# Kernel tuning notes

Measured on AMD Instinct MI355X. Metric: run time of the kernel, lower is better.

The kernel has to match this reference:

```python
import jax, jax.numpy as jnp
import numpy as np

B, S, E, H, MLP = 2, 2048, 1024, 16, 4096
VEC = 8          # args.vec_length: block-row height of vector-sparse mask
SPARSITY = 0.9   # fraction of attention entries dropped
D = E // H


def _make_mask():
    # static_random_mask_aligned: each block-row of VEC query rows keeps a
    # random ~(1-sparsity) subset of key columns. Diagonal kept so every
    # softmax row is non-empty.
    rng = np.random.default_rng(0)
    block = rng.random((S // VEC, S)) < (1.0 - SPARSITY)   # [m, n]
    mask = np.repeat(block, VEC, axis=0)                   # [S, S]
    mask |= np.eye(S, dtype=bool)
    return jnp.asarray(mask)


def setup_inputs() -> dict:
    key = jax.random.key(0)
    ks = jax.random.split(key, 8)
    w = lambda k, shp: (0.02 * jax.random.normal(k, shp, dtype=jnp.float32))
    return {
        "x": jax.random.normal(ks[0], (B, S, E), dtype=jnp.float32),
        "mask": _make_mask(),                       # [S,S] bool, static
        "w_qkv": w(ks[1], (3 * E, E)),             # in_proj_weight
        "b_qkv": jnp.zeros((3 * E,), jnp.float32),
        "w_out": w(ks[2], (E, E)),                 # out_proj
        "b_out": jnp.zeros((E,), jnp.float32),
        "g1": jnp.ones((E,), jnp.float32), "beta1": jnp.zeros((E,), jnp.float32),
        "g2": jnp.ones((E,), jnp.float32), "beta2": jnp.zeros((E,), jnp.float32),
        "w1": w(ks[3], (MLP, E)), "bias1": jnp.zeros((MLP,), jnp.float32),
        "w2": w(ks[4], (E, MLP)), "bias2": jnp.zeros((E,), jnp.float32),
    }


def _layer_norm(x, g, b, eps=1e-5):
    mu = jnp.mean(x, axis=-1, keepdims=True)
    var = jnp.mean(jnp.square(x - mu), axis=-1, keepdims=True)
    return (x - mu) * jax.lax.rsqrt(var + eps) * g + b


def _sparse_mha(h, mask, w_qkv, b_qkv, w_out, b_out):
    qkv = jnp.einsum("bse,fe->bsf", h, w_qkv) + b_qkv       # [B,S,3E]
    q, k, v = jnp.split(qkv, 3, axis=-1)
    q = q.reshape(B, S, H, D)
    k = k.reshape(B, S, H, D)
    v = v.reshape(B, S, H, D)
    scores = jnp.einsum("bqhd,bkhd->bhqk", q, k) / jnp.sqrt(jnp.float32(D))
    scores = jnp.where(mask[None, None], scores, jnp.float32(-1e9))
    p = jax.nn.softmax(scores, axis=-1)
    ctx = jnp.einsum("bhqk,bkhd->bqhd", p, v).reshape(B, S, E)
    return jnp.einsum("bse,fe->bsf", ctx, w_out) + b_out


def reference(x, mask, w_qkv, b_qkv, w_out, b_out, g1, beta1, g2, beta2,
              w1, bias1, w2, bias2):
    h = _layer_norm(x, g1, beta1)
    attn = _sparse_mha(h, mask, w_qkv, b_qkv, w_out, b_out)
    out = attn + x                      # residual 1
    out = _layer_norm(out, g2, beta2)
    out = jnp.einsum("bse,me->bsm", out, w1) + bias1   # linear1 (no activation, as in source)
    out = jnp.einsum("bsm,em->bse", out, w2) + bias2   # linear2
    return out + x                      # residual adds ORIGINAL x (as in source)
```

## Files before the change

### kernel.cpp

```cpp
#include <hip/hip_runtime.h>
#include <cstdint>
#include <cstddef>

typedef unsigned short u16;
typedef unsigned int u32;
typedef unsigned long long u64;
typedef short s16x8 __attribute__((ext_vector_type(8)));
typedef float f32x4 __attribute__((ext_vector_type(4)));
typedef _Float16 f16x4 __attribute__((ext_vector_type(4)));
typedef _Float16 f16x8 __attribute__((ext_vector_type(8)));

#define S_LEN 2048
#define EMB   1024
#define NHEAD 16
#define HD    64
#define E3    3072
#define MLPD  4096
#define NROWS 4096
#define LCAP  640

__device__ __forceinline__ float bf2f(u16 v) {
  union { u32 i; float f; } c; c.i = ((u32)v) << 16; return c.f;
}
__device__ __forceinline__ u16 f2bf(float f) {
  union { float f; u32 i; } c; c.f = f;
  u32 x = c.i;
  return (u16)((x + 0x7FFFu + ((x >> 16) & 1u)) >> 16);
}
__device__ __forceinline__ u16 f2h(float f) {
  _Float16 h = (_Float16)f;
  union { _Float16 h; u16 b; } c; c.h = h; return c.b;
}

__device__ __forceinline__ void gl2lds16(const void* g, void* l) {
  __builtin_amdgcn_global_load_lds(
      (__attribute__((address_space(1))) void*)(g),
      (__attribute__((address_space(3))) void*)(l), 16, 0, 0);
}

__global__ void detect_flags(const u32* __restrict__ w1s, int* __restrict__ dtflag,
                             const u32* __restrict__ mask, int* __restrict__ maskrep) {
  __shared__ int hits[256];
  __shared__ u32 red[256];
  int h = 0; u32 v = 0;
  for (int i = threadIdx.x; i < 4096; i += 256) {
    u32 w = w1s[i];
    if ((w & 0xFFFFu) && (((w >> 7) & 0xFFu) >= 0xC8u)) ++h;
    v |= mask[i];
  }
  hits[threadIdx.x] = h; red[threadIdx.x] = v;
  __syncthreads();
  if (threadIdx.x == 0) {
    int t = 0; u32 o = 0;
    for (int i = 0; i < 256; ++i) { t += hits[i]; o |= red[i]; }
    *dtflag = (t > 8) ? 1 : 0;
    int rep;
    if (o <= 1u) rep = 0;
    else if (o & 0x80u) rep = 1;
    else if (o & 0x00800000u) rep = 2;
    else rep = 3;
    *maskrep = rep;
  }
}

__device__ __forceinline__ bool maskbit(const void* m, int rep, size_t idx) {
  switch (rep) {
    case 0:  return ((const int*)m)[idx] != 0;
    case 1:  return ((const u16*)m)[idx] != 0;
    case 2:  return ((const u32*)m)[idx] != 0;
    default: return ((const unsigned char*)m)[idx] != 0;
  }
}

__global__ __launch_bounds__(256)
void cvt_kernel(const void* __restrict__ src, u16* __restrict__ dst,
                int n8, const int* __restrict__ dtflag) {
  const int i = blockIdx.x * blockDim.x + threadIdx.x;
  if (i >= n8) return;
  if (*dtflag) {
    const float4 a = ((const float4*)src)[i * 2];
    const float4 b = ((const float4*)src)[i * 2 + 1];
    u16 o[8] = {f2bf(a.x), f2bf(a.y), f2bf(a.z), f2bf(a.w),
                f2bf(b.x), f2bf(b.y), f2bf(b.z), f2bf(b.w)};
    *(uint4*)(dst + (size_t)i * 8) = *(const uint4*)o;
  } else {
    ((uint4*)dst)[i] = ((const uint4*)src)[i];
  }
}

__global__ void cvt_small(const void* s0, u16* d0, const void* s1, u16* d1,
                          const void* s2, u16* d2, const void* s3, u16* d3,
                          const void* s4, u16* d4, const void* s5, u16* d5,
                          const void* s6, u16* d6, const void* s7, u16* d7,
                          const int* __restrict__ dtflag) {
  const int f = *dtflag;
  const void* srcs[8] = {s0, s1, s2, s3, s4, s5, s6, s7};
  u16* dsts[8] = {d0, d1, d2, d3, d4, d5, d6, d7};
  const int ns[8] = {E3, EMB, EMB, EMB, EMB, EMB, MLPD, EMB};
#pragma unroll
  for (int k = 0; k < 8; ++k) {
    for (int idx = threadIdx.x; idx < ns[k]; idx += 256)
      dsts[k][idx] = f ? f2bf(((const float*)srcs[k])[idx])
                       : ((const u16*)srcs[k])[idx];
  }
}

__global__ void build_lists(const void* __restrict__ mask, const int* __restrict__ repf,
                            int* __restrict__ lists, int* __restrict__ cnt,
                            unsigned char* __restrict__ diagflag) {
  __shared__ int num;
  const int m = blockIdx.x;
  if (threadIdx.x == 0) num = 0;
  __syncthreads();
  const int rep = *repf;
  const int row0 = m * 8;
  for (int j = threadIdx.x; j < S_LEN; j += 256) {
    int srcrow = (j == row0) ? (row0 + 1) : row0;
    bool bit = maskbit(mask, rep, (size_t)srcrow * S_LEN + j);
    if (j >= row0 && j < row0 + 8) diagflag[j] = bit ? 0 : 1;
    if (bit) {
      int p = atomicAdd(&num, 1);
      if (p < LCAP) lists[m * LCAP + p] = j * 256;
    }
  }
  __syncthreads();
  if (threadIdx.x == 0) cnt[m] = (num < LCAP) ? num : LCAP;
}

__global__ __launch_bounds__(256)
void ln_kernel(const void* __restrict__ Xv, const u16* __restrict__ g,
               const u16* __restrict__ be, u16* __restrict__ O,
               const int* __restrict__ inf32) {
  const int wv = threadIdx.x >> 6, ln = threadIdx.x & 63;
  const int row = blockIdx.x * 4 + wv;
  float v[16];
  if (inf32 && *inf32) {
    const float* xr = (const float*)Xv + (size_t)row * EMB;
    float4 a0 = *(const float4*)(xr + ln * 8);
    float4 a1 = *(const float4*)(xr + ln * 8 + 4);
    float4 b0 = *(const float4*)(xr + 512 + ln * 8);
    float4 b1 = *(const float4*)(xr + 512 + ln * 8 + 4);
    v[0]=a0.x; v[1]=a0.y; v[2]=a0.z; v[3]=a0.w; v[4]=a1.x; v[5]=a1.y; v[6]=a1.z; v[7]=a1.w;
    v[8]=b0.x; v[9]=b0.y; v[10]=b0.z; v[11]=b0.w; v[12]=b1.x; v[13]=b1.y; v[14]=b1.z; v[15]=b1.w;
  } else {
    const u16* xr = (const u16*)Xv + (size_t)row * EMB;
    union { uint4 u; u16 s[8]; } p0, p1;
    p0.u = *(const uint4*)(xr + ln * 8);
    p1.u = *(const uint4*)(xr + 512 + ln * 8);
#pragma unroll
    for (int t = 0; t < 8; ++t) { v[t] = bf2f(p0.s[t]); v[8 + t] = bf2f(p1.s[t]); }
  }
  float s = 0.f, sq = 0.f;
#pragma unroll
  for (int t = 0; t < 16; ++t) { s += v[t]; sq += v[t] * v[t]; }
#pragma unroll
  for (int off = 32; off; off >>= 1) { s += __shfl_xor(s, off); sq += __shfl_xor(sq, off); }
  const float mu = s * (1.0f / EMB);
  const float var = sq * (1.0f / EMB) - mu * mu;
  const float rsig = rsqrtf(var + 1e-5f);
  union { uint4 u; u16 s[8]; } g0, g1v, b0, b1v, o0, o1;
  g0.u = *(const uint4*)(g + ln * 8);   g1v.u = *(const uint4*)(g + 512 + ln * 8);
  b0.u = *(const uint4*)(be + ln * 8);  b1v.u = *(const uint4*)(be + 512 + ln * 8);
#pragma unroll
  for (int t = 0; t < 8; ++t) {
    o0.s[t] = f2bf((v[t]     - mu) * rsig * bf2f(g0.s[t])  + bf2f(b0.s[t]));
    o1.s[t] = f2bf((v[8 + t] - mu) * rsig * bf2f(g1v.s[t]) + bf2f(b1v.s[t]));
  }
  u16* orow = O + (size_t)row * EMB;
  *(uint4*)(orow + ln * 8) = o0.u;
  *(uint4*)(orow + 512 + ln * 8) = o1.u;
}

__global__ __launch_bounds__(256)
void gemm_bt(const u16* __restrict__ A, const u16* __restrict__ B,
             const u16* __restrict__ bias, u16* __restrict__ C,
             int M, int N, int K) {
  __shared__ u16 a_sh[128 * 64];
  __shared__ u16 b_sh[128 * 64];
  const int tid = threadIdx.x;
  const int wv = tid >> 6, ln = tid & 63;
  const int wm = wv & 1, wn = wv >> 1;
  const int tm = blockIdx.y, tn = blockIdx.x;
  const int srow = ln >> 3;
  const int scol = ((ln & 7) ^ srow) * 8;
  const int q = ln >> 4, rr = ln & 15;

  f32x4 acc[4][4] = {};
  const u16* Abase = A + (size_t)(tm * 128) * K;
  const u16* Bbase = B + (size_t)(tn * 128) * K;

  for (int k0 = 0; k0 < K; k0 += 64) {
    __syncthreads();
#pragma unroll
    for (int c = 0; c < 4; ++c) {
      const int chunk = wv * 4 + c;
      const int row = chunk * 8 + srow;
      gl2lds16(Abase + (size_t)row * K + k0 + scol, &a_sh[chunk * 512]);
      gl2lds16(Bbase + (size_t)row * K + k0 + scol, &b_sh[chunk * 512]);
    }
    __syncthreads();
#pragma unroll
    for (int kk = 0; kk < 2; ++kk) {
      const int slot = ((kk * 4 + q) ^ (rr & 7)) * 8;
      s16x8 af[4], bfr[4];
#pragma unroll
      for (int mi = 0; mi < 4; ++mi)
        af[mi] = *(const s16x8*)&a_sh[(wm * 64 + mi * 16 + rr) * 64 + slot];
#pragma unroll
      for (int ni = 0; ni < 4; ++ni)
        bfr[ni] = *(const s16x8*)&b_sh[(wn * 64 + ni * 16 + rr) * 64 + slot];
#pragma unroll
      for (int mi = 0; mi < 4; ++mi)
#pragma unroll
        for (int ni = 0; ni < 4; ++ni)
          acc[mi][ni] = __builtin_amdgcn_mfma_f32_16x16x32_bf16(af[mi], bfr[ni], acc[mi][ni], 0, 0, 0);
    }
  }
#pragma unroll
  for (int ni = 0; ni < 4; ++ni) {
    const int col = tn * 128 + wn * 64 + ni * 16 + rr;
    const float bv = bf2f(bias[col]);
#pragma unroll
    for (int mi = 0; mi < 4; ++mi)
#pragma unroll
      for (int r2 = 0; r2 < 4; ++r2) {
        const int row = tm * 128 + wm * 64 + mi * 16 + q * 4 + r2;
        C[(size_t)row * N + col] = f2bf(acc[mi][ni][r2] + bv);
      }
  }
}

__global__ __launch_bounds__(256)
void gemm_bt_sk(const u16* __restrict__ A, const u16* __restrict__ B,
                u16* __restrict__ P0, u16* __restrict__ P1,
                int M, int N, int K) {
  __shared__ u16 a_sh[128 * 64];
  __shared__ u16 b_sh[128 * 64];
  const int tid = threadIdx.x;
  const int wv = tid >> 6, ln = tid & 63;
  const int wm = wv & 1, wn = wv >> 1;
  const int tm = blockIdx.y, tn = blockIdx.x, kz = blockIdx.z;
  const int Kh = K >> 1;
  const int koff = kz * Kh;
  const int srow = ln >> 3;
  const int scol = ((ln & 7) ^ srow) * 8;
  const int q = ln >> 4, rr = ln & 15;

  f32x4 acc[4][4] = {};
  const u16* Abase = A + (size_t)(tm * 128) * K + koff;
  const u16* Bbase = B + (size_t)(tn * 128) * K + koff;

  for (int k0 = 0; k0 < Kh; k0 += 64) {
    __syncthreads();
#pragma unroll
    for (int c = 0; c < 4; ++c) {
      const int chunk = wv * 4 + c;
      const int row = chunk * 8 + srow;
      gl2lds16(Abase + (size_t)row * K + k0 + scol, &a_sh[chunk * 512]);
      gl2lds16(Bbase + (size_t)row * K + k0 + scol, &b_sh[chunk * 512]);
    }
    __syncthreads();
#pragma unroll
    for (int kk = 0; kk < 2; ++kk) {
      const int slot = ((kk * 4 + q) ^ (rr & 7)) * 8;
      s16x8 af[4], bfr[4];
#pragma unroll
      for (int mi = 0; mi < 4; ++mi)
        af[mi] = *(const s16x8*)&a_sh[(wm * 64 + mi * 16 + rr) * 64 + slot];
#pragma unroll
      for (int ni = 0; ni < 4; ++ni)
        bfr[ni] = *(const s16x8*)&b_sh[(wn * 64 + ni * 16 + rr) * 64 + slot];
#pragma unroll
      for (int mi = 0; mi < 4; ++mi)
#pragma unroll
        for (int ni = 0; ni < 4; ++ni)
          acc[mi][ni] = __builtin_amdgcn_mfma_f32_16x16x32_bf16(af[mi], bfr[ni], acc[mi][ni], 0, 0, 0);
    }
  }
  u16* P = kz ? P1 : P0;
#pragma unroll
  for (int ni = 0; ni < 4; ++ni) {
    const int col = tn * 128 + wn * 64 + ni * 16 + rr;
#pragma unroll
    for (int mi = 0; mi < 4; ++mi)
#pragma unroll
      for (int r2 = 0; r2 < 4; ++r2) {
        const int row = tm * 128 + wm * 64 + mi * 16 + q * 4 + r2;
        P[(size_t)row * N + col] = f2bf(acc[mi][ni][r2]);
      }
  }
}

__global__ __launch_bounds__(256)
void combine_kernel(const u16* __restrict__ P0, const u16* __restrict__ P1,
                    const u16* __restrict__ bias, const void* __restrict__ xr,
                    void* __restrict__ Ov, const int* __restrict__ f32io) {
  const int i = blockIdx.x * 256 + threadIdx.x;
  const int col8 = (i & 127) * 8;
  union { uint4 u; u16 s[8]; } a, b, bi;
  a.u = ((const uint4*)P0)[i];
  b.u = ((const uint4*)P1)[i];
  bi.u = *(const uint4*)(bias + col8);
  const int f = *f32io;
  float o[8];
#pragma unroll
  for (int t = 0; t < 8; ++t) o[t] = bf2f(a.s[t]) + bf2f(b.s[t]) + bf2f(bi.s[t]);
  if (f) {
    const float4 x0 = ((const float4*)xr)[i * 2];
    const float4 x1 = ((const float4*)xr)[i * 2 + 1];
    o[0]+=x0.x; o[1]+=x0.y; o[2]+=x0.z; o[3]+=x0.w;
    o[4]+=x1.x; o[5]+=x1.y; o[6]+=x1.z; o[7]+=x1.w;
    float4 r0 = {o[0],o[1],o[2],o[3]}, r1 = {o[4],o[5],o[6],o[7]};
    ((float4*)Ov)[i * 2] = r0;
    ((float4*)Ov)[i * 2 + 1] = r1;
  } else {
    union { uint4 u; u16 s[8]; } xv;
    xv.u = ((const uint4*)xr)[i];
    u16 r[8];
#pragma unroll
    for (int t = 0; t < 8; ++t) r[t] = f2bf(o[t] + bf2f(xv.s[t]));
    ((uint4*)Ov)[i] = *(const uint4*)r;
  }
}

__global__ __launch_bounds__(256)
void gemm_qkv(const u16* __restrict__ A, const u16* __restrict__ B,
              const u16* __restrict__ bias,
              u16* __restrict__ Qb, u16* __restrict__ KVp,
              int K) {
  __shared__ u16 a_sh[128 * 64];
  __shared__ u16 b_sh[128 * 64];
  const int tid = threadIdx.x;
  const int wv = tid >> 6, ln = tid & 63;
  const int wm = wv & 1, wn = wv >> 1;
  const int tm = blockIdx.y, tn = blockIdx.x;
  const int srow = ln >> 3;
  const int scol = ((ln & 7) ^ srow) * 8;
  const int q = ln >> 4, rr = ln & 15;

  f32x4 acc[4][4] = {};
  const u16* Abase = A + (size_t)(tm * 128) * K;
  const u16* Bbase = B + (size_t)(tn * 128) * K;

  for (int k0 = 0; k0 < K; k0 += 64) {
    __syncthreads();
#pragma unroll
    for (int c = 0; c < 4; ++c) {
      const int chunk = wv * 4 + c;
      const int row = chunk * 8 + srow;
      gl2lds16(Abase + (size_t)row * K + k0 + scol, &a_sh[chunk * 512]);
      gl2lds16(Bbase + (size_t)row * K + k0 + scol, &b_sh[chunk * 512]);
    }
    __syncthreads();
#pragma unroll
    for (int kk = 0; kk < 2; ++kk) {
      const int slot = ((kk * 4 + q) ^ (rr & 7)) * 8;
      s16x8 af[4], bfr[4];
#pragma unroll
      for (int mi = 0; mi < 4; ++mi)
        af[mi] = *(const s16x8*)&a_sh[(wm * 64 + mi * 16 + rr) * 64 + slot];
#pragma unroll
      for (int ni = 0; ni < 4; ++ni)
        bfr[ni] = *(const s16x8*)&b_sh[(wn * 64 + ni * 16 + rr) * 64 + slot];
#pragma unroll
      for (int mi = 0; mi < 4; ++mi)
#pragma unroll
        for (int ni = 0; ni < 4; ++ni)
          acc[mi][ni] = __builtin_amdgcn_mfma_f32_16x16x32_bf16(af[mi], bfr[ni], acc[mi][ni], 0, 0, 0);
    }
  }
  const int third = (tn * 128) >> 10;
  const float QS = 0.125f * 1.44269504f;
#pragma unroll
  for (int ni = 0; ni < 4; ++ni) {
    const int col = tn * 128 + wn * 64 + ni * 16 + rr;
    const int w = col & 1023;
    const float bv = bf2f(bias[col]);
#pragma unroll
    for (int mi = 0; mi < 4; ++mi)
#pragma unroll
      for (int r2 = 0; r2 < 4; ++r2) {
        const int row = tm * 128 + wm * 64 + mi * 16 + q * 4 + r2;
        const float o = acc[mi][ni][r2] + bv;
        if (third == 0) {
          Qb[(size_t)row * 1024 + w] = f2h(o * QS);
        } else {
          const int hh = w >> 6, d = w & 63;
          const int bq_ = row >> 11, s = row & 2047;
          KVp[((size_t)(bq_ * NHEAD + hh) * S_LEN + s) * 128 +
              ((third == 1) ? 0 : 64) + d] = f2h(o);
        }
      }
  }
}

__global__ __launch_bounds__(256)
void gemm_bt_n64(const u16* __restrict__ A, const u16* __restrict__ B,
                 const u16* __restrict__ bias, const void* __restrict__ resid,
                 void* __restrict__ Cv, int M, int N, int K,
                 const int* __restrict__ residf32, const int* __restrict__ outf32) {
  __shared__ u16 a_sh[128 * 64];
  __shared__ u16 b_sh[64 * 64];
  const int tid = threadIdx.x;
  const int wv = tid >> 6, ln = tid & 63;
  const int wm = wv & 1, wn = wv >> 1;
  const int tm = blockIdx.y, tn = blockIdx.x;
  const int srow = ln >> 3;
  const int scol = ((ln & 7) ^ srow) * 8;
  const int q = ln >> 4, rr = ln & 15;

  f32x4 acc[4][2] = {};
  const u16* Abase = A + (size_t)(tm * 128) * K;
  const u16* Bbase = B + (size_t)(tn * 64) * K;

  for (int k0 = 0; k0 < K; k0 += 64) {
    __syncthreads();
#pragma unroll
    for (int c = 0; c < 4; ++c) {
      const int chunk = wv * 4 + c;
      const int row = chunk * 8 + srow;
      gl2lds16(Abase + (size_t)row * K + k0 + scol, &a_sh[chunk * 512]);
    }
#pragma unroll
    for (int c = 0; c < 2; ++c) {
      const int chunk = wv * 2 + c;
      const int row = chunk * 8 + srow;
      gl2lds16(Bbase + (size_t)row * K + k0 + scol, &b_sh[chunk * 512]);
    }
    __syncthreads();
#pragma unroll
    for (int kk = 0; kk < 2; ++kk) {
      const int slot = ((kk * 4 + q) ^ (rr & 7)) * 8;
      s16x8 af[4], bfr[2];
#pragma unroll
      for (int mi = 0; mi < 4; ++mi)
        af[mi] = *(const s16x8*)&a_sh[(wm * 64 + mi * 16 + rr) * 64 + slot];
#pragma unroll
      for (int ni = 0; ni < 2; ++ni)
        bfr[ni] = *(const s16x8*)&b_sh[(wn * 32 + ni * 16 + rr) * 64 + slot];
#pragma unroll
      for (int mi = 0; mi < 4; ++mi)
#pragma unroll
        for (int ni = 0; ni < 2; ++ni)
          acc[mi][ni] = __builtin_amdgcn_mfma_f32_16x16x32_bf16(af[mi], bfr[ni], acc[mi][ni], 0, 0, 0);
    }
  }
  const int rf32 = residf32 ? *residf32 : 0;
  const int f32o = outf32 ? *outf32 : 0;
#pragma unroll
  for (int ni = 0; ni < 2; ++ni) {
    const int col = tn * 64 + wn * 32 + ni * 16 + rr;
    const float bv = bf2f(bias[col]);
#pragma unroll
    for (int mi = 0; mi < 4; ++mi)
#pragma unroll
      for (int r2 = 0; r2 < 4; ++r2) {
        const int row = tm * 128 + wm * 64 + mi * 16 + q * 4 + r2;
        const size_t idx = (size_t)row * N + col;
        float o = acc[mi][ni][r2] + bv;
        if (resid)
          o += rf32 ? ((const float*)resid)[idx] : bf2f(((const u16*)resid)[idx]);
        if (f32o) ((float*)Cv)[idx] = o;
        else      ((u16*)Cv)[idx] = f2bf(o);
      }
  }
}

__global__ __launch_bounds__(256)
void attn_kernel(const u16* __restrict__ Qb, const u16* __restrict__ KVp,
                 const int* __restrict__ lists,
                 const int* __restrict__ cnt, const unsigned char* __restrict__ diagflag,
                 u16* __restrict__ ctx) {
  __shared__ int list_sh[4][LCAP];
  __shared__ uint4 vsh4[4][128];
  const int g = blockIdx.x;
  const int bh = g & 31;
  const int mq = g >> 5;
  const int b = bh >> 4, h = bh & 15;
  const int tid = threadIdx.x, wv = tid >> 6, ln = tid & 63;
  const int lg = ln >> 4;
  const int dl = ln & 15;
  const int m = mq * 4 + wv;
  const int i0 = m * 8;

#pragma unroll
  for (int w = 0; w < 4; ++w) {
    const int nw = cnt[mq * 4 + w];
    for (int e = tid; e < nw; e += 256) list_sh[w][e] = lists[(mq * 4 + w) * LCAP + e];
  }
  __syncthreads();

  const int n = cnt[m];
  const u64 du = *(const u64*)(diagflag + i0);

  f16x8 qb0 = {}, qb1 = {};
  if (dl < 8) {
    const u16* qr = Qb + (size_t)(b * S_LEN + i0 + dl) * EMB + h * 64 + lg * 8;
    union { uint4 u; f16x8 h; } a0, a1;
    a0.u = *(const uint4*)qr;
    a1.u = *(const uint4*)(qr + 32);
    qb0 = a0.h; qb1 = a1.h;
  }

  const char* kvb = (const char*)KVp + (size_t)bh * S_LEN * 256;

  uint4* vwp = &vsh4[wv][0];
  const int widx = ((lg >> 1) << 5) + ((dl & 3) << 3) + ((dl >> 2) << 1) + (lg & 1);
  const u16* vrp = (const u16*)vwp + (lg << 4) + dl;

  float rs = 0.f;
  f32x4 acc[4] = {};

  auto CHUNK = [&](int c0, int mode) {
    int le;
    if (mode == 2) {
      le = (i0 + (dl & 7)) * 256;
    } else {
      const int e = c0 + dl;
      const int idx = (mode == 1 && e >= n) ? 0 : e;
      le = list_sh[wv][idx];
    }
    const char* base = kvb + le + (lg << 4);
    union { uint4 u; f16x8 h; } ka0, ka1;
    ka0.u = *(const uint4*)(base);
    ka1.u = *(const uint4*)(base + 64);
    const uint4 v0 = *(const uint4*)(base + 128);
    const uint4 v1 = *(const uint4*)(base + 192);

    f32x4 st = {};
    st = __builtin_amdgcn_mfma_f32_16x16x32_f16(ka0.h, qb0, st, 0, 0, 0);
    st = __builtin_amdgcn_mfma_f32_16x16x32_f16(ka1.h, qb1, st, 0, 0, 0);

    vwp[widx] = v0;
    vwp[widx + 64] = v1;

    _Float16 ph[4];
#pragma unroll
    for (int r = 0; r < 4; ++r) {
      float s = st[r];
      s = fminf(fmaxf(s, -126.f), 15.f);
      float p = exp2f(s);
      bool keep = true;
      const int e2 = (lg << 2) + r;
      if (mode == 1) keep = (c0 + e2) < n;
      if (mode == 2) keep = (e2 == dl) && (((du >> ((e2 & 7) * 8)) & 1ull) != 0ull);
      p = keep ? p : 0.f;
      ph[r] = (_Float16)p;
      rs += (float)ph[r];
    }
    const f16x4 pa = { ph[0], ph[1], ph[2], ph[3] };

#pragma unroll
    for (int dc = 0; dc < 4; ++dc) {
      union { u16 s[4]; f16x4 h; } bf;
      bf.s[0] = vrp[dc * 256 +   0];
      bf.s[1] = vrp[dc * 256 +  64];
      bf.s[2] = vrp[dc * 256 + 128];
      bf.s[3] = vrp[dc * 256 + 192];
      acc[dc] = __builtin_amdgcn_mfma_f32_16x16x16f16(pa, bf.h, acc[dc], 0, 0, 0);
    }
  };

  int c0 = 0;
  for (; c0 + 16 <= n; c0 += 16) CHUNK(c0, 0);
  if (c0 < n) CHUNK(c0, 1);
  CHUNK(0, 2);

  rs += __shfl_xor(rs, 16);
  rs += __shfl_xor(rs, 32);

  float invs[4];
#pragma unroll
  for (int r = 0; r < 4; ++r) invs[r] = __shfl(rs, (lg << 2) + r);

  if (lg < 2) {
#pragma unroll
    for (int r = 0; r < 4; ++r) {
      const float inv = 1.0f / invs[r];
      u16* orow = ctx + (size_t)(b * S_LEN + i0 + (lg << 2) + r) * EMB + h * 64 + dl;
#pragma unroll
      for (int dc = 0; dc < 4; ++dc)
        orow[dc * 16] = f2bf(acc[dc][r] * inv);
    }
  }
}

extern "C" void kernel_launch(void* const* d_in, const int* in_sizes, int n_in,
                              void* d_out, int out_size, void* d_ws, size_t ws_size,
                              hipStream_t stream) {
  const void* x_raw    = d_in[0];
  const void* mask     = d_in[1];
  const void* wqkv_raw = d_in[2];
  const void* bqkv_raw = d_in[3];
  const void* wout_raw = d_in[4];
  const void* bout_raw = d_in[5];
  const void* g1_raw   = d_in[6];
  const void* be1_raw  = d_in[7];
  const void* g2_raw   = d_in[8];
  const void* be2_raw  = d_in[9];
  const void* w1_raw   = d_in[10];
  const void* b1_raw   = d_in[11];
  const void* w2_raw   = d_in[12];
  const void* b2_raw   = d_in[13];

  char* ws = (char*)d_ws;
  const size_t MB = 1u << 20;
  int* dtflag         = (int*)ws;
  int* maskrep        = (int*)(ws + 64);
  int* cnt            = (int*)(ws + 1024);
  unsigned char* dfl  = (unsigned char*)(ws + 4096);
  int* lists          = (int*)(ws + 8192);
  u16* R1  = (u16*)(ws + 1 * MB);
  u16* Qb  = (u16*)(ws + 9 * MB);
  u16* KVp = (u16*)(ws + 17 * MB);
  u16* M1  = (u16*)(ws + 17 * MB);
  u16* W   = (u16*)(ws + 49 * MB);
  char* sm = ws + 57 * MB;
  u16* bq  = (u16*)(sm);
  u16* bo  = (u16*)(sm + 8192);
  u16* g1b = (u16*)(sm + 16384);
  u16* be1b= (u16*)(sm + 24576);
  u16* g2b = (u16*)(sm + 32768);
  u16* be2b= (u16*)(sm + 40960);
  u16* b1b = (u16*)(sm + 49152);
  u16* b2b = (u16*)(sm + 65536);

  detect_flags<<<dim3(1), dim3(256), 0, stream>>>((const u32*)w1_raw, dtflag,
                                                  (const u32*)mask, maskrep);
  build_lists<<<dim3(256), dim3(256), 0, stream>>>(mask, maskrep, lists, cnt, dfl);
  cvt_small<<<dim3(1), dim3(256), 0, stream>>>(
      bqkv_raw, bq, bout_raw, bo, g1_raw, g1b, be1_raw, be1b,
      g2_raw, g2b, be2_raw, be2b, b1_raw, b1b, b2_raw, b2b, dtflag);

  auto cvt = [&](const void* src, u16* dst, int n) {
    const int n8 = n / 8;
    cvt_kernel<<<dim3((n8 + 255) / 256), dim3(256), 0, stream>>>(src, dst, n8, dtflag);
  };

  ln_kernel<<<dim3(NROWS / 4), dim3(256), 0, stream>>>(x_raw, g1b, be1b, R1, dtflag);
  cvt(wqkv_raw, W, E3 * EMB);
  gemm_qkv<<<dim3(E3 / 128, NROWS / 128), dim3(256), 0, stream>>>(
      R1, W, bq, Qb, KVp, EMB);
  attn_kernel<<<dim3(2 * NHEAD * 64), dim3(256), 0, stream>>>(
      Qb, KVp, lists, cnt, dfl, R1);
  cvt(wout_raw, W, EMB * EMB);
  gemm_bt_n64<<<dim3(EMB / 64, NROWS / 128), dim3(256), 0, stream>>>(
      R1, W, bo, x_raw, Qb, NROWS, EMB, EMB, dtflag, nullptr);
  ln_kernel<<<dim3(NROWS / 4), dim3(256), 0, stream>>>(Qb, g2b, be2b, R1, nullptr);
  cvt(w1_raw, W, MLPD * EMB);
  gemm_bt<<<dim3(MLPD / 128, NROWS / 128), dim3(256), 0, stream>>>(
      R1, W, b1b, M1, NROWS, MLPD, EMB);
  cvt(w2_raw, W, EMB * MLPD);
  gemm_bt_sk<<<dim3(EMB / 128, NROWS / 128, 2), dim3(256), 0, stream>>>(
      M1, W, R1, Qb, NROWS, EMB, MLPD);
  combine_kernel<<<dim3(NROWS * EMB / 8 / 256), dim3(256), 0, stream>>>(
      R1, Qb, b2b, x_raw, d_out, dtflag);
}
```

Measured before the change: 411.6 us.

## Software-pipeline sparse attention gathers with double-buffered swizzled V tiles

Restructures the attention chunk loop so the K/V gather for the next 16-key chunk is issued into registers before the current chunk's MFMAs run. The V tile is double-buffered in LDS with a new swizzled layout, which removes the load-to-use stall on each scattered global read. Key lists are stored as 16-bit indices with a smaller cap, and a 6-waves occupancy hint is added, both to shrink LDS and raise residency. The trade-off is higher register pressure from the prefetch registers, and the kernel now assumes no block-row has more than 320 kept keys.

```diff
diff --git a/kernel.cpp b/kernel.cpp
--- a/kernel.cpp
+++ b/kernel.cpp
@@ -17,7 +17,7 @@
 #define E3    3072
 #define MLPD  4096
 #define NROWS 4096
-#define LCAP  640
+#define LCAP  320
 
 __device__ __forceinline__ float bf2f(u16 v) {
   union { u32 i; float f; } c; c.i = ((u32)v) << 16; return c.f;
@@ -466,13 +466,13 @@
   }
 }
 
-__global__ __launch_bounds__(256)
+__global__ __launch_bounds__(256, 6)
 void attn_kernel(const u16* __restrict__ Qb, const u16* __restrict__ KVp,
                  const int* __restrict__ lists,
                  const int* __restrict__ cnt, const unsigned char* __restrict__ diagflag,
                  u16* __restrict__ ctx) {
-  __shared__ int list_sh[4][LCAP];
-  __shared__ uint4 vsh4[4][128];
+  __shared__ u16 list_sh[4][LCAP];
+  __shared__ uint4 vsh4[4][2][128];
   const int g = blockIdx.x;
   const int bh = g & 31;
   const int mq = g >> 5;
@@ -486,7 +486,8 @@
 #pragma unroll
   for (int w = 0; w < 4; ++w) {
     const int nw = cnt[mq * 4 + w];
-    for (int e = tid; e < nw; e += 256) list_sh[w][e] = lists[(mq * 4 + w) * LCAP + e];
+    for (int e = tid; e < nw; e += 256)
+      list_sh[w][e] = (u16)((u32)lists[(mq * 4 + w) * LCAP + e] >> 8);
   }
   __syncthreads();
 
@@ -504,67 +505,99 @@
 
   const char* kvb = (const char*)KVp + (size_t)bh * S_LEN * 256;
 
-  uint4* vwp = &vsh4[wv][0];
-  const int widx = ((lg >> 1) << 5) + ((dl & 3) << 3) + ((dl >> 2) << 1) + (lg & 1);
-  const u16* vrp = (const u16*)vwp + (lg << 4) + dl;
+  const int wslab = ((dl >> 2) & 1)
+                  + ((((dl >> 1) & 1) ^ (dl >> 3)) << 1)
+                  + (((dl & 1) ^ (lg & 1)) << 2)
+                  + ((dl >> 3) << 3)
+                  + ((lg & 1) << 4)
+                  + (((lg >> 1) & 1) << 5);
+  const int c3l = lg >> 1, o0l = dl >> 3;
+  const int LB = ((lg & 1) << 3) + (c3l << 6) + (o0l << 7) + (dl & 7);
+  const int tm0 = ((0 ^ c3l) << 4) + ((0 ^ o0l) << 5);
+  const int tm1 = ((0 ^ c3l) << 4) + ((1 ^ o0l) << 5);
+  const int tm2 = ((1 ^ c3l) << 4) + ((1 ^ o0l) << 5) - ((1 ^ o0l) << 5) + ((0 ^ o0l) << 5);
+  const int tm3 = ((1 ^ c3l) << 4) + ((1 ^ o0l) << 5);
+  const u16* vtile = (const u16*)&vsh4[wv][0][0];
 
   float rs = 0.f;
   f32x4 acc[4] = {};
-
-  auto CHUNK = [&](int c0, int mode) {
+  const int T = ((n + 15) >> 4) + 1;
+
+  auto kaddr = [&](int ci) -> const char* {
     int le;
-    if (mode == 2) {
-      le = (i0 + (dl & 7)) * 256;
+    if (ci >= T - 1) {
+      le = (i0 + (dl & 7)) << 8;
     } else {
-      const int e = c0 + dl;
-      const int idx = (mode == 1 && e >= n) ? 0 : e;
-      le = list_sh[wv][idx];
-    }
-    const char* base = kvb + le + (lg << 4);
-    union { uint4 u; f16x8 h; } ka0, ka1;
-    ka0.u = *(const uint4*)(base);
-    ka1.u = *(const uint4*)(base + 64);
-    const uint4 v0 = *(const uint4*)(base + 128);
-    const uint4 v1 = *(const uint4*)(base + 192);
-
+      const int e = ci * 16 + dl;
+      le = ((int)list_sh[wv][(e < n) ? e : 0]) << 8;
+    }
+    return kvb + le + (lg << 4);
+  };
+
+  uint4 ka0, ka1;
+  {
+    const char* p0 = kaddr(0);
+    ka0 = *(const uint4*)p0;
+    ka1 = *(const uint4*)(p0 + 64);
+    const uint4 w0 = *(const uint4*)(p0 + 128);
+    const uint4 w1 = *(const uint4*)(p0 + 192);
+    vsh4[wv][0][wslab] = w0;
+    vsh4[wv][0][wslab + 64] = w1;
+  }
+
+  for (int ci = 0; ci < T; ++ci) {
+    const int par = ci & 1;
+    const bool more = (ci + 1 < T);
+    uint4 na0, na1, nv0, nv1;
+    if (more) {
+      const char* pn = kaddr(ci + 1);
+      na0 = *(const uint4*)pn;
+      na1 = *(const uint4*)(pn + 64);
+      nv0 = *(const uint4*)(pn + 128);
+      nv1 = *(const uint4*)(pn + 192);
+    }
+
+    union { uint4 u; f16x8 h; } kc0, kc1;
+    kc0.u = ka0; kc1.u = ka1;
     f32x4 st = {};
-    st = __builtin_amdgcn_mfma_f32_16x16x32_f16(ka0.h, qb0, st, 0, 0, 0);
-    st = __builtin_amdgcn_mfma_f32_16x16x32_f16(ka1.h, qb1, st, 0, 0, 0);
-
-    vwp[widx] = v0;
-    vwp[widx + 64] = v1;
-
+    st = __builtin_amdgcn_mfma_f32_16x16x32_f16(kc0.h, qb0, st, 0, 0, 0);
+    st = __builtin_amdgcn_mfma_f32_16x16x32_f16(kc1.h, qb1, st, 0, 0, 0);
+
+    const bool isdiag = (ci == T - 1);
+    const int cbase = ci * 16;
     _Float16 ph[4];
 #pragma unroll
     for (int r = 0; r < 4; ++r) {
       float s = st[r];
       s = fminf(fmaxf(s, -126.f), 15.f);
       float p = exp2f(s);
-      bool keep = true;
       const int e2 = (lg << 2) + r;
-      if (mode == 1) keep = (c0 + e2) < n;
-      if (mode == 2) keep = (e2 == dl) && (((du >> ((e2 & 7) * 8)) & 1ull) != 0ull);
+      bool keep;
+      if (isdiag) keep = (e2 == dl) && (((du >> ((e2 & 7) * 8)) & 1ull) != 0ull);
+      else        keep = (cbase + e2) < n;
       p = keep ? p : 0.f;
       ph[r] = (_Float16)p;
-      rs += (float)ph[r];
+      rs += p;
     }
     const f16x4 pa = { ph[0], ph[1], ph[2], ph[3] };
 
+    const u16* vrp = vtile + (par << 10);
 #pragma unroll
     for (int dc = 0; dc < 4; ++dc) {
       union { u16 s[4]; f16x4 h; } bf;
-      bf.s[0] = vrp[dc * 256 +   0];
-      bf.s[1] = vrp[dc * 256 +  64];
-      bf.s[2] = vrp[dc * 256 + 128];
-      bf.s[3] = vrp[dc * 256 + 192];
+      bf.s[0] = vrp[LB + tm0 + dc * 256];
+      bf.s[1] = vrp[LB + tm1 + dc * 256];
+      bf.s[2] = vrp[LB + tm2 + dc * 256];
+      bf.s[3] = vrp[LB + tm3 + dc * 256];
       acc[dc] = __builtin_amdgcn_mfma_f32_16x16x16f16(pa, bf.h, acc[dc], 0, 0, 0);
     }
-  };
-
-  int c0 = 0;
-  for (; c0 + 16 <= n; c0 += 16) CHUNK(c0, 0);
-  if (c0 < n) CHUNK(c0, 1);
-  CHUNK(0, 2);
+
+    if (more) {
+      vsh4[wv][par ^ 1][wslab] = nv0;
+      vsh4[wv][par ^ 1][wslab + 64] = nv1;
+      ka0 = na0; ka1 = na1;
+    }
+  }
 
   rs += __shfl_xor(rs, 16);
   rs += __shfl_xor(rs, 32);
```

Result: slower. 422.1 us (+2.5%).
